# Kernel optimization log

Hardware: AMD Instinct MI355X
Metric: run time of the kernel (lower is better)

The kernel has to match this reference:

```python
import jax, jax.numpy as jnp
import numpy as np

BOS = 1
NUM_LAYERS = 2
HID = 1024
VOCAB = 32000
SEQ = 64


def setup_inputs() -> dict:
    key = jax.random.key(0)
    ks = jax.random.split(key, 16)
    s = 0.02  # weight scale
    return {
        "src": jax.random.randint(ks[0], (SEQ,), 0, VOCAB),
        "tgt": jax.random.randint(ks[1], (SEQ,), 0, VOCAB),
        "emb_enc": jax.random.normal(ks[2], (VOCAB, HID), jnp.float32) * s,
        "enc_Wih": jax.random.normal(ks[3], (NUM_LAYERS, 4 * HID, HID), jnp.float32) * s,
        "enc_Whh": jax.random.normal(ks[4], (NUM_LAYERS, 4 * HID, HID), jnp.float32) * s,
        "enc_bih": jax.random.normal(ks[5], (NUM_LAYERS, 4 * HID), jnp.float32) * s,
        "enc_bhh": jax.random.normal(ks[6], (NUM_LAYERS, 4 * HID), jnp.float32) * s,
        "emb_dec": jax.random.normal(ks[7], (VOCAB, HID), jnp.float32) * s,
        "dec_Wih": jax.random.normal(ks[8], (NUM_LAYERS, 4 * HID, HID), jnp.float32) * s,
        "dec_Whh": jax.random.normal(ks[9], (NUM_LAYERS, 4 * HID, HID), jnp.float32) * s,
        "dec_bih": jax.random.normal(ks[10], (NUM_LAYERS, 4 * HID), jnp.float32) * s,
        "dec_bhh": jax.random.normal(ks[11], (NUM_LAYERS, 4 * HID), jnp.float32) * s,
        "out_W": jax.random.normal(ks[12], (VOCAB, HID), jnp.float32) * s,
        "out_b": jax.random.normal(ks[13], (VOCAB,), jnp.float32) * s,
    }


def _lstm_stack_step(Wih, Whh, bih, bhh, x, h, c):
    # x: [H]; h, c: [L, H]. PyTorch gate order: i, f, g, o.
    new_h, new_c = [], []
    inp = x
    for l in range(Wih.shape[0]):
        g = Wih[l] @ inp + bih[l] + Whh[l] @ h[l] + bhh[l]  # [4H]
        gi, gf, gg, go = jnp.split(g, 4)
        i = jax.nn.sigmoid(gi)
        f = jax.nn.sigmoid(gf)
        cand = jnp.tanh(gg)
        o = jax.nn.sigmoid(go)
        c_l = f * c[l] + i * cand
        h_l = o * jnp.tanh(c_l)
        new_h.append(h_l)
        new_c.append(c_l)
        inp = h_l
    return jnp.stack(new_h), jnp.stack(new_c)


def reference(src, tgt, emb_enc, enc_Wih, enc_Whh, enc_bih, enc_bhh,
              emb_dec, dec_Wih, dec_Whh, dec_bih, dec_bhh, out_W, out_b):
    h0 = jnp.zeros((NUM_LAYERS, HID), jnp.float32)
    c0 = jnp.zeros((NUM_LAYERS, HID), jnp.float32)

    # ---- encoder: seq-major, batch=1 ----
    def enc_step(carry, tok):
        h, c = carry
        x = emb_enc[tok]
        h, c = _lstm_stack_step(enc_Wih, enc_Whh, enc_bih, enc_bhh, x, h, c)
        return (h, c), h[-1]

    (h, c), encoder_outputs = jax.lax.scan(enc_step, (h0, c0), src)

    def dec_step(carry, _):
        h, c, tok = carry
        x = emb_dec[tok]
        h, c = _lstm_stack_step(dec_Wih, dec_Whh, dec_bih, dec_bhh, x, h, c)
        logp = jax.nn.log_softmax(out_W @ h[-1] + out_b)  # [V]
        nxt = jnp.argmax(logp)
        return (h, c, nxt), logp

    tgt_len = tgt.shape[0]
    (_, _, _), dec_logps = jax.lax.scan(
        dec_step, (h, c, jnp.asarray(BOS, src.dtype)), None, length=tgt_len)
    return dec_logps  # [T, V]
```

## Files before the change

### kernel.cpp

```cpp
#include <hip/hip_runtime.h>
#include <math.h>

#define HID    1024
#define G4     4096
#define VOC    32000
#define SEQL   64
#define BOSTOK 1
#define NBLK   256
#define NTHR   1024
#define NWAVES (NTHR / 64)
#define TOTW   (NBLK * NWAVES)

struct P {
  const int*   src;
  const float* embE; const float* eWih; const float* eWhh; const float* ebih; const float* ebhh;
  const float* embD; const float* dWih; const float* dWhh; const float* dbih; const float* dbhh;
  const float* oW;   const float* ob;
  float* out;
  float* ws;
};

__device__ __forceinline__ float gld(const float* p) {
  return __hip_atomic_load((float*)p, __ATOMIC_RELAXED, __HIP_MEMORY_SCOPE_AGENT);
}
__device__ __forceinline__ void gst(float* p, float v) {
  __hip_atomic_store(p, v, __ATOMIC_RELAXED, __HIP_MEMORY_SCOPE_AGENT);
}
__device__ __forceinline__ int gldi(const int* p) {
  return __hip_atomic_load((int*)p, __ATOMIC_RELAXED, __HIP_MEMORY_SCOPE_AGENT);
}
__device__ __forceinline__ void gsti(int* p, int v) {
  __hip_atomic_store(p, v, __ATOMIC_RELAXED, __HIP_MEMORY_SCOPE_AGENT);
}

__device__ __forceinline__ void gridbar(unsigned* cnt, unsigned* gen) {
  __syncthreads();
  if (threadIdx.x == 0) {
    __builtin_amdgcn_s_waitcnt(0);
    unsigned g = __hip_atomic_load(gen, __ATOMIC_RELAXED, __HIP_MEMORY_SCOPE_AGENT);
    unsigned a = __hip_atomic_fetch_add(cnt, 1u, __ATOMIC_ACQ_REL, __HIP_MEMORY_SCOPE_AGENT);
    if (a == NBLK - 1) {
      __hip_atomic_store(cnt, 0u, __ATOMIC_RELAXED, __HIP_MEMORY_SCOPE_AGENT);
      __hip_atomic_fetch_add(gen, 1u, __ATOMIC_RELEASE, __HIP_MEMORY_SCOPE_AGENT);
    } else {
      while (__hip_atomic_load(gen, __ATOMIC_RELAXED, __HIP_MEMORY_SCOPE_AGENT) == g)
        __builtin_amdgcn_s_sleep(8);
      (void)__hip_atomic_load(gen, __ATOMIC_ACQUIRE, __HIP_MEMORY_SCOPE_AGENT);
    }
  }
  __syncthreads();
}

__device__ __forceinline__ float wsum(float v) {
#pragma unroll
  for (int o = 32; o > 0; o >>= 1) v += __shfl_xor(v, o, 64);
  return v;
}

__device__ __forceinline__ float dotg(const float* __restrict__ w, const float* v, int lane) {
  const float4* w4 = (const float4*)w;
  const float4* v4 = (const float4*)v;
  float acc = 0.f;
#pragma unroll
  for (int j = 0; j < 4; ++j) {
    float4 a = w4[lane + 64 * j];
    float4 b = v4[lane + 64 * j];
    acc += a.x * b.x + a.y * b.y + a.z * b.z + a.w * b.w;
  }
  return acc;
}

__device__ __forceinline__ void derive(const float* __restrict__ pa, const float* __restrict__ cin,
                                       float* __restrict__ cout, float* __restrict__ hout, int tid) {
  float gi = gld(pa + tid), gf = gld(pa + HID + tid);
  float gg = gld(pa + 2 * HID + tid), go = gld(pa + 3 * HID + tid);
  float c  = cin ? gld(cin + tid) : 0.f;
  float si = 1.f / (1.f + expf(-gi));
  float sf = 1.f / (1.f + expf(-gf));
  float so = 1.f / (1.f + expf(-go));
  float cn = sf * c + si * tanhf(gg);
  hout[tid] = so * tanhf(cn);
  if (cout) gst(cout + tid, cn);
}

__global__ void init_bar(unsigned* bar) { bar[0] = 0; bar[1] = 0; }

__global__ void __launch_bounds__(NTHR) rnn_all(P p) {
  const int  tid  = threadIdx.x;
  const int  lane = tid & 63;
  const int  wv   = tid >> 6;
  const int  gw   = blockIdx.x * NWAVES + wv;
  const bool b0   = (blockIdx.x == 0);

  unsigned* cnt = (unsigned*)p.ws;
  unsigned* gen = cnt + 1;

  __shared__ __align__(16) float sx[HID];
  __shared__ __align__(16) float sh0[HID];
  __shared__ __align__(16) float sh1[HID];
  __shared__ float rv[NWAVES];
  __shared__ int   ri[NWAVES];
  __shared__ int   stok;

  float* pa0e = p.ws + 64;
  float* pa1e = pa0e + 4 * G4;
  float* pa0d = pa1e + 4 * G4;
  float* pa1d = pa0d + 4 * G4;
  float* c0e  = pa1d + 4 * G4;
  float* c1e  = c0e + 4 * HID;
  float* c0d  = c1e + 4 * HID;
  float* c1d  = c0d + 4 * HID;
  float* B0   = c1d + 4 * HID;
  float* B1   = B0 + G4;
  float* pmv  = B1 + G4;
  int*   pmi  = (int*)(pmv + NBLK);
  float* lsep = (float*)(pmi + NBLK);

  const float* eW0i = p.eWih;  const float* eW1i = p.eWih + (size_t)G4 * HID;
  const float* eW0h = p.eWhh;  const float* eW1h = p.eWhh + (size_t)G4 * HID;
  const float* eb0i = p.ebih;  const float* eb1i = p.ebih + G4;
  const float* eb0h = p.ebhh;  const float* eb1h = p.ebhh + G4;
  const float* dW0i = p.dWih;  const float* dW1i = p.dWih + (size_t)G4 * HID;
  const float* dW0h = p.dWhh;  const float* dW1h = p.dWhh + (size_t)G4 * HID;
  const float* db0i = p.dbih;  const float* db1i = p.dbih + G4;
  const float* db0h = p.dbhh;  const float* db1h = p.dbhh + G4;

  for (int k = 0; k <= SEQL; ++k) {
    if (k < SEQL) {
      int tok = p.src[k];
      sx[tid] = p.embE[(size_t)tok * HID + tid];
    }
    if (k >= 1) {
      derive(pa0e + ((k - 1) & 3) * G4,
             (k >= 2) ? (c0e + ((k - 1) & 3) * HID) : nullptr,
             b0 ? (c0e + (k & 3) * HID) : nullptr, sh0, tid);
    } else sh0[tid] = 0.f;
    if (k >= 2) {
      derive(pa1e + ((k - 2) & 3) * G4,
             (k >= 3) ? (c1e + ((k - 2) & 3) * HID) : nullptr,
             b0 ? (c1e + ((k - 1) & 3) * HID) : nullptr, sh1, tid);
    } else sh1[tid] = 0.f;
    __syncthreads();

    for (int it = gw; it < 2 * G4; it += TOTW) {
      if (it < G4) {
        if (k < SEQL) {
          int r = it;
          float a = dotg(eW0i + (size_t)r * HID, sx, lane) +
                    dotg(eW0h + (size_t)r * HID, sh0, lane);
          float v = wsum(a) + eb0i[r] + eb0h[r];
          if (lane == 0) gst(pa0e + (k & 3) * G4 + r, v);
        }
      } else if (k >= 1) {
        int r = it - G4;
        float a = dotg(eW1i + (size_t)r * HID, sh0, lane) +
                  dotg(eW1h + (size_t)r * HID, sh1, lane);
        float v = wsum(a) + eb1i[r] + eb1h[r];
        if (lane == 0) gst(pa1e + ((k - 1) & 3) * G4 + r, v);
      }
    }
    gridbar(cnt, gen);
  }

  {
    derive(pa0e + (63 & 3) * G4, c0e + (63 & 3) * HID, b0 ? (c0d + 0) : nullptr, sh0, tid);
    derive(pa1e + (63 & 3) * G4, c1e + (63 & 3) * HID, b0 ? (c1d + 0) : nullptr, sh1, tid);
    __syncthreads();
    for (int it = gw; it < 2 * G4; it += TOTW) {
      if (it < G4) {
        int r = it;
        float v = wsum(dotg(dW0h + (size_t)r * HID, sh0, lane)) + db0i[r] + db0h[r];
        if (lane == 0) gst(B0 + r, v);
      } else {
        int r = it - G4;
        float v = wsum(dotg(dW1h + (size_t)r * HID, sh1, lane)) + db1i[r] + db1h[r];
        if (lane == 0) gst(B1 + r, v);
      }
    }
    gridbar(cnt, gen);
  }

  for (int t = 0; t < SEQL; ++t) {
    if (t == 0) {
      if (tid == 0) stok = BOSTOK;
    } else if (wv == 0) {
      float bv = -1e30f; int bi = 0;
#pragma unroll
      for (int j = 0; j < NBLK / 64; ++j) {
        int   idx = lane + 64 * j;
        float v   = gld(pmv + idx);
        int   i2  = gldi(pmi + idx);
        if (v > bv || (v == bv && i2 < bi)) { bv = v; bi = i2; }
      }
#pragma unroll
      for (int o = 32; o > 0; o >>= 1) {
        float v  = __shfl_xor(bv, o, 64);
        int   i2 = __shfl_xor(bi, o, 64);
        if (v > bv || (v == bv && i2 < bi)) { bv = v; bi = i2; }
      }
      if (lane == 0) stok = bi;
    }
    __syncthreads();
    sx[tid] = p.embD[(size_t)stok * HID + tid];
    __syncthreads();
    for (int it = gw; it < G4; it += TOTW) {
      float v = wsum(dotg(dW0i + (size_t)it * HID, sx, lane)) + gld(B0 + it);
      if (lane == 0) gst(pa0d + (t & 3) * G4 + it, v);
    }
    gridbar(cnt, gen);

    derive(pa0d + (t & 3) * G4, c0d + (t & 3) * HID,
           b0 ? (c0d + ((t + 1) & 3) * HID) : nullptr, sh0, tid);
    __syncthreads();
    for (int it = gw; it < G4; it += TOTW) {
      float v = wsum(dotg(dW1i + (size_t)it * HID, sh0, lane)) + gld(B1 + it);
      if (lane == 0) gst(pa1d + (t & 3) * G4 + it, v);
    }
    gridbar(cnt, gen);

    derive(pa1d + (t & 3) * G4, c1d + (t & 3) * HID,
           b0 ? (c1d + ((t + 1) & 3) * HID) : nullptr, sh1, tid);
    __syncthreads();
    float bv = -1e30f; int bi = 0;
    for (int it = gw; it < VOC + 2 * G4; it += TOTW) {
      if (it < VOC) {
        float v = wsum(dotg(p.oW + (size_t)it * HID, sh1, lane)) + p.ob[it];
        if (lane == 0) gst(p.out + (size_t)t * VOC + it, v);
        if (v > bv) { bv = v; bi = it; }
      } else if (it < VOC + G4) {
        int r = it - VOC;
        float v = wsum(dotg(dW0h + (size_t)r * HID, sh0, lane)) + db0i[r] + db0h[r];
        if (lane == 0) gst(B0 + r, v);
      } else {
        int r = it - VOC - G4;
        float v = wsum(dotg(dW1h + (size_t)r * HID, sh1, lane)) + db1i[r] + db1h[r];
        if (lane == 0) gst(B1 + r, v);
      }
    }
    if (lane == 0) { rv[wv] = bv; ri[wv] = bi; }
    __syncthreads();
    if (tid == 0) {
      float v = rv[0]; int i2 = ri[0];
      for (int j = 1; j < NWAVES; ++j)
        if (rv[j] > v || (rv[j] == v && ri[j] < i2)) { v = rv[j]; i2 = ri[j]; }
      gst(pmv + blockIdx.x, v); gsti(pmi + blockIdx.x, i2);
    }
    gridbar(cnt, gen);
  }

  {
    const int row = blockIdx.x >> 2;
    const int seg = blockIdx.x & 3;
    float* base = p.out + (size_t)row * VOC + (size_t)seg * 8000;

    float lm = -1e30f;
    for (int i = tid; i < 8000; i += NTHR) lm = fmaxf(lm, gld(base + i));
#pragma unroll
    for (int o = 32; o > 0; o >>= 1) lm = fmaxf(lm, __shfl_xor(lm, o, 64));
    if (lane == 0) rv[wv] = lm;
    __syncthreads();
    float bm = rv[0];
#pragma unroll
    for (int j = 1; j < NWAVES; ++j) bm = fmaxf(bm, rv[j]);
    float ls = 0.f;
    for (int i = tid; i < 8000; i += NTHR) ls += expf(gld(base + i) - bm);
    ls = wsum(ls);
    __syncthreads();
    if (lane == 0) rv[wv] = ls;
    __syncthreads();
    if (tid == 0) {
      float ss = 0.f;
      for (int j = 0; j < NWAVES; ++j) ss += rv[j];
      gst(lsep + blockIdx.x * 2,     bm);
      gst(lsep + blockIdx.x * 2 + 1, ss);
    }
    gridbar(cnt, gen);

    const float* lp = lsep + (size_t)row * 8;
    float l0 = gld(lp), l2 = gld(lp + 2), l4 = gld(lp + 4), l6 = gld(lp + 6);
    float s1 = gld(lp + 1), s3 = gld(lp + 3), s5 = gld(lp + 5), s7 = gld(lp + 7);
    float M = fmaxf(fmaxf(l0, l2), fmaxf(l4, l6));
    float S = s1 * expf(l0 - M) + s3 * expf(l2 - M) +
              s5 * expf(l4 - M) + s7 * expf(l6 - M);
    float L = M + logf(S);
    for (int i = tid; i < 8000; i += NTHR) base[i] = gld(base + i) - L;
  }
}

extern "C" void kernel_launch(void* const* d_in, const int* in_sizes, int n_in,
                              void* d_out, int out_size, void* d_ws, size_t ws_size,
                              hipStream_t stream) {
  P p;
  p.src  = (const int*)d_in[0];
  p.embE = (const float*)d_in[2];
  p.eWih = (const float*)d_in[3];
  p.eWhh = (const float*)d_in[4];
  p.ebih = (const float*)d_in[5];
  p.ebhh = (const float*)d_in[6];
  p.embD = (const float*)d_in[7];
  p.dWih = (const float*)d_in[8];
  p.dWhh = (const float*)d_in[9];
  p.dbih = (const float*)d_in[10];
  p.dbhh = (const float*)d_in[11];
  p.oW   = (const float*)d_in[12];
  p.ob   = (const float*)d_in[13];
  p.out  = (float*)d_out;
  p.ws   = (float*)d_ws;

  hipLaunchKernelGGL(init_bar, dim3(1), dim3(1), 0, stream, (unsigned*)d_ws);
  void* args[] = { &p };
  hipLaunchCooperativeKernel((const void*)rnn_all, dim3(NBLK), dim3(NTHR), args, 0, stream);
}
```

Before: 8.213 ms.

## Use hierarchical grid barrier and occupancy-sized grid of smaller blocks

Replaces the single-counter grid barrier with a two-level barrier: blocks first arrive at per-group counters, then the last arrival of each group bumps a top-level counter, and release flags are padded across cache lines. Block size drops to 512 threads and the grid is sized from the occupancy query, up to 1024 blocks, so more waves share the weight GEMVs across CUs. The goal is less atomic contention at the roughly 200 grid barriers and higher memory-level parallelism. The cost is more blocks taking part in every barrier, a host-side occupancy query whose result is cached, and generalized softmax segmenting.

```diff
diff --git a/kernel.cpp b/kernel.cpp
--- a/kernel.cpp
+++ b/kernel.cpp
@@ -6,10 +6,10 @@
 #define VOC    32000
 #define SEQL   64
 #define BOSTOK 1
-#define NBLK   256
-#define NTHR   1024
+#define NTHR   512
 #define NWAVES (NTHR / 64)
-#define TOTW   (NBLK * NWAVES)
+#define NGRP   32
+#define BARW   4096
 
 struct P {
   const int*   src;
@@ -33,19 +33,29 @@
   __hip_atomic_store(p, v, __ATOMIC_RELAXED, __HIP_MEMORY_SCOPE_AGENT);
 }
 
-__device__ __forceinline__ void gridbar(unsigned* cnt, unsigned* gen) {
+__device__ __forceinline__ void gridbar(unsigned* bar, unsigned phase, int g, unsigned grpsz) {
   __syncthreads();
   if (threadIdx.x == 0) {
     __builtin_amdgcn_s_waitcnt(0);
-    unsigned g = __hip_atomic_load(gen, __ATOMIC_RELAXED, __HIP_MEMORY_SCOPE_AGENT);
-    unsigned a = __hip_atomic_fetch_add(cnt, 1u, __ATOMIC_ACQ_REL, __HIP_MEMORY_SCOPE_AGENT);
-    if (a == NBLK - 1) {
-      __hip_atomic_store(cnt, 0u, __ATOMIC_RELAXED, __HIP_MEMORY_SCOPE_AGENT);
-      __hip_atomic_fetch_add(gen, 1u, __ATOMIC_RELEASE, __HIP_MEMORY_SCOPE_AGENT);
-    } else {
-      while (__hip_atomic_load(gen, __ATOMIC_RELAXED, __HIP_MEMORY_SCOPE_AGENT) == g)
-        __builtin_amdgcn_s_sleep(8);
-      (void)__hip_atomic_load(gen, __ATOMIC_ACQUIRE, __HIP_MEMORY_SCOPE_AGENT);
+    unsigned* grpc = bar + 64 + 32 * g;
+    unsigned* topc = bar + 32;
+    bool released = false;
+    unsigned a = __hip_atomic_fetch_add(grpc, 1u, __ATOMIC_ACQ_REL, __HIP_MEMORY_SCOPE_AGENT);
+    if (a == phase * grpsz - 1u) {
+      unsigned b = __hip_atomic_fetch_add(topc, 1u, __ATOMIC_ACQ_REL, __HIP_MEMORY_SCOPE_AGENT);
+      if (b == phase * NGRP - 1u) {
+#pragma unroll
+        for (int g2 = 0; g2 < NGRP; ++g2)
+          __hip_atomic_store(bar + 2048 + 32 * g2, phase,
+                             __ATOMIC_RELEASE, __HIP_MEMORY_SCOPE_AGENT);
+        released = true;
+      }
+    }
+    if (!released) {
+      unsigned* gg = bar + 2048 + 32 * g;
+      while (__hip_atomic_load(gg, __ATOMIC_RELAXED, __HIP_MEMORY_SCOPE_AGENT) < phase)
+        __builtin_amdgcn_s_sleep(4);
+      (void)__hip_atomic_load(gg, __ATOMIC_ACQUIRE, __HIP_MEMORY_SCOPE_AGENT);
     }
   }
   __syncthreads();
@@ -72,28 +82,39 @@
 
 __device__ __forceinline__ void derive(const float* __restrict__ pa, const float* __restrict__ cin,
                                        float* __restrict__ cout, float* __restrict__ hout, int tid) {
-  float gi = gld(pa + tid), gf = gld(pa + HID + tid);
-  float gg = gld(pa + 2 * HID + tid), go = gld(pa + 3 * HID + tid);
-  float c  = cin ? gld(cin + tid) : 0.f;
-  float si = 1.f / (1.f + expf(-gi));
-  float sf = 1.f / (1.f + expf(-gf));
-  float so = 1.f / (1.f + expf(-go));
-  float cn = sf * c + si * tanhf(gg);
-  hout[tid] = so * tanhf(cn);
-  if (cout) gst(cout + tid, cn);
-}
-
-__global__ void init_bar(unsigned* bar) { bar[0] = 0; bar[1] = 0; }
-
-__global__ void __launch_bounds__(NTHR) rnn_all(P p) {
-  const int  tid  = threadIdx.x;
-  const int  lane = tid & 63;
-  const int  wv   = tid >> 6;
-  const int  gw   = blockIdx.x * NWAVES + wv;
-  const bool b0   = (blockIdx.x == 0);
-
-  unsigned* cnt = (unsigned*)p.ws;
-  unsigned* gen = cnt + 1;
+  for (int i = tid; i < HID; i += NTHR) {
+    float gi = gld(pa + i), gf = gld(pa + HID + i);
+    float gg = gld(pa + 2 * HID + i), go = gld(pa + 3 * HID + i);
+    float c  = cin ? gld(cin + i) : 0.f;
+    float si = 1.f / (1.f + expf(-gi));
+    float sf = 1.f / (1.f + expf(-gf));
+    float so = 1.f / (1.f + expf(-go));
+    float cn = sf * c + si * tanhf(gg);
+    hout[i] = so * tanhf(cn);
+    if (cout) gst(cout + i, cn);
+  }
+}
+
+__device__ __forceinline__ void zerov(float* h, int tid) {
+  for (int i = tid; i < HID; i += NTHR) h[i] = 0.f;
+}
+
+__global__ void init_bar(unsigned* bar) {
+  for (int i = threadIdx.x; i < BARW; i += 256) bar[i] = 0;
+}
+
+__global__ void __launch_bounds__(NTHR, 8) rnn_all(P p) {
+  const int  tid   = threadIdx.x;
+  const int  lane  = tid & 63;
+  const int  wv    = tid >> 6;
+  const int  nblk  = gridDim.x;
+  const int  totw  = nblk * NWAVES;
+  const int  gw    = blockIdx.x * NWAVES + wv;
+  const int  grp   = blockIdx.x & (NGRP - 1);
+  const unsigned grpsz = (unsigned)(nblk / NGRP);
+  const bool b0    = (blockIdx.x == 0);
+  unsigned   ph    = 0;
+  unsigned*  bar   = (unsigned*)p.ws;
 
   __shared__ __align__(16) float sx[HID];
   __shared__ __align__(16) float sh0[HID];
@@ -102,7 +123,7 @@
   __shared__ int   ri[NWAVES];
   __shared__ int   stok;
 
-  float* pa0e = p.ws + 64;
+  float* pa0e = p.ws + BARW;
   float* pa1e = pa0e + 4 * G4;
   float* pa0d = pa1e + 4 * G4;
   float* pa1d = pa0d + 4 * G4;
@@ -113,8 +134,8 @@
   float* B0   = c1d + 4 * HID;
   float* B1   = B0 + G4;
   float* pmv  = B1 + G4;
-  int*   pmi  = (int*)(pmv + NBLK);
-  float* lsep = (float*)(pmi + NBLK);
+  int*   pmi  = (int*)(pmv + 1024);
+  float* lsep = (float*)(pmi + 1024);
 
   const float* eW0i = p.eWih;  const float* eW1i = p.eWih + (size_t)G4 * HID;
   const float* eW0h = p.eWhh;  const float* eW1h = p.eWhh + (size_t)G4 * HID;
@@ -128,21 +149,21 @@
   for (int k = 0; k <= SEQL; ++k) {
     if (k < SEQL) {
       int tok = p.src[k];
-      sx[tid] = p.embE[(size_t)tok * HID + tid];
+      for (int i = tid; i < HID; i += NTHR) sx[i] = p.embE[(size_t)tok * HID + i];
     }
     if (k >= 1) {
       derive(pa0e + ((k - 1) & 3) * G4,
              (k >= 2) ? (c0e + ((k - 1) & 3) * HID) : nullptr,
              b0 ? (c0e + (k & 3) * HID) : nullptr, sh0, tid);
-    } else sh0[tid] = 0.f;
+    } else zerov(sh0, tid);
     if (k >= 2) {
       derive(pa1e + ((k - 2) & 3) * G4,
              (k >= 3) ? (c1e + ((k - 2) & 3) * HID) : nullptr,
              b0 ? (c1e + ((k - 1) & 3) * HID) : nullptr, sh1, tid);
-    } else sh1[tid] = 0.f;
-    __syncthreads();
-
-    for (int it = gw; it < 2 * G4; it += TOTW) {
+    } else zerov(sh1, tid);
+    __syncthreads();
+
+    for (int it = gw; it < 2 * G4; it += totw) {
       if (it < G4) {
         if (k < SEQL) {
           int r = it;
@@ -159,14 +180,14 @@
         if (lane == 0) gst(pa1e + ((k - 1) & 3) * G4 + r, v);
       }
     }
-    gridbar(cnt, gen);
+    gridbar(bar, ++ph, grp, grpsz);
   }
 
   {
     derive(pa0e + (63 & 3) * G4, c0e + (63 & 3) * HID, b0 ? (c0d + 0) : nullptr, sh0, tid);
     derive(pa1e + (63 & 3) * G4, c1e + (63 & 3) * HID, b0 ? (c1d + 0) : nullptr, sh1, tid);
     __syncthreads();
-    for (int it = gw; it < 2 * G4; it += TOTW) {
+    for (int it = gw; it < 2 * G4; it += totw) {
       if (it < G4) {
         int r = it;
         float v = wsum(dotg(dW0h + (size_t)r * HID, sh0, lane)) + db0i[r] + db0h[r];
@@ -177,7 +198,7 @@
         if (lane == 0) gst(B1 + r, v);
       }
     }
-    gridbar(cnt, gen);
+    gridbar(bar, ++ph, grp, grpsz);
   }
 
   for (int t = 0; t < SEQL; ++t) {
@@ -185,11 +206,9 @@
       if (tid == 0) stok = BOSTOK;
     } else if (wv == 0) {
       float bv = -1e30f; int bi = 0;
-#pragma unroll
-      for (int j = 0; j < NBLK / 64; ++j) {
-        int   idx = lane + 64 * j;
-        float v   = gld(pmv + idx);
-        int   i2  = gldi(pmi + idx);
+      for (int idx = lane; idx < nblk; idx += 64) {
+        float v  = gld(pmv + idx);
+        int   i2 = gldi(pmi + idx);
         if (v > bv || (v == bv && i2 < bi)) { bv = v; bi = i2; }
       }
 #pragma unroll
@@ -201,28 +220,31 @@
       if (lane == 0) stok = bi;
     }
     __syncthreads();
-    sx[tid] = p.embD[(size_t)stok * HID + tid];
-    __syncthreads();
-    for (int it = gw; it < G4; it += TOTW) {
+    {
+      int tok = stok;
+      for (int i = tid; i < HID; i += NTHR) sx[i] = p.embD[(size_t)tok * HID + i];
+    }
+    __syncthreads();
+    for (int it = gw; it < G4; it += totw) {
       float v = wsum(dotg(dW0i + (size_t)it * HID, sx, lane)) + gld(B0 + it);
       if (lane == 0) gst(pa0d + (t & 3) * G4 + it, v);
     }
-    gridbar(cnt, gen);
+    gridbar(bar, ++ph, grp, grpsz);
 
     derive(pa0d + (t & 3) * G4, c0d + (t & 3) * HID,
            b0 ? (c0d + ((t + 1) & 3) * HID) : nullptr, sh0, tid);
     __syncthreads();
-    for (int it = gw; it < G4; it += TOTW) {
+    for (int it = gw; it < G4; it += totw) {
       float v = wsum(dotg(dW1i + (size_t)it * HID, sh0, lane)) + gld(B1 + it);
       if (lane == 0) gst(pa1d + (t & 3) * G4 + it, v);
     }
-    gridbar(cnt, gen);
+    gridbar(bar, ++ph, grp, grpsz);
 
     derive(pa1d + (t & 3) * G4, c1d + (t & 3) * HID,
            b0 ? (c1d + ((t + 1) & 3) * HID) : nullptr, sh1, tid);
     __syncthreads();
     float bv = -1e30f; int bi = 0;
-    for (int it = gw; it < VOC + 2 * G4; it += TOTW) {
+    for (int it = gw; it < VOC + 2 * G4; it += totw) {
       if (it < VOC) {
         float v = wsum(dotg(p.oW + (size_t)it * HID, sh1, lane)) + p.ob[it];
         if (lane == 0) gst(p.out + (size_t)t * VOC + it, v);
@@ -245,16 +267,19 @@
         if (rv[j] > v || (rv[j] == v && ri[j] < i2)) { v = rv[j]; i2 = ri[j]; }
       gst(pmv + blockIdx.x, v); gsti(pmi + blockIdx.x, i2);
     }
-    gridbar(cnt, gen);
+    gridbar(bar, ++ph, grp, grpsz);
   }
 
   {
-    const int row = blockIdx.x >> 2;
-    const int seg = blockIdx.x & 3;
-    float* base = p.out + (size_t)row * VOC + (size_t)seg * 8000;
+    const int spr  = nblk >> 6;
+    const int lg   = (spr == 4) ? 2 : (spr == 8) ? 3 : 4;
+    const int row  = blockIdx.x >> lg;
+    const int seg  = blockIdx.x & (spr - 1);
+    const int slen = VOC >> lg;
+    float* base = p.out + (size_t)row * VOC + (size_t)seg * slen;
 
     float lm = -1e30f;
-    for (int i = tid; i < 8000; i += NTHR) lm = fmaxf(lm, gld(base + i));
+    for (int i = tid; i < slen; i += NTHR) lm = fmaxf(lm, gld(base + i));
 #pragma unroll
     for (int o = 32; o > 0; o >>= 1) lm = fmaxf(lm, __shfl_xor(lm, o, 64));
     if (lane == 0) rv[wv] = lm;
@@ -263,7 +288,7 @@
 #pragma unroll
     for (int j = 1; j < NWAVES; ++j) bm = fmaxf(bm, rv[j]);
     float ls = 0.f;
-    for (int i = tid; i < 8000; i += NTHR) ls += expf(gld(base + i) - bm);
+    for (int i = tid; i < slen; i += NTHR) ls += expf(gld(base + i) - bm);
     ls = wsum(ls);
     __syncthreads();
     if (lane == 0) rv[wv] = ls;
@@ -274,16 +299,15 @@
       gst(lsep + blockIdx.x * 2,     bm);
       gst(lsep + blockIdx.x * 2 + 1, ss);
     }
-    gridbar(cnt, gen);
-
-    const float* lp = lsep + (size_t)row * 8;
-    float l0 = gld(lp), l2 = gld(lp + 2), l4 = gld(lp + 4), l6 = gld(lp + 6);
-    float s1 = gld(lp + 1), s3 = gld(lp + 3), s5 = gld(lp + 5), s7 = gld(lp + 7);
-    float M = fmaxf(fmaxf(l0, l2), fmaxf(l4, l6));
-    float S = s1 * expf(l0 - M) + s3 * expf(l2 - M) +
-              s5 * expf(l4 - M) + s7 * expf(l6 - M);
+    gridbar(bar, ++ph, grp, grpsz);
+
+    const float* lp = lsep + (size_t)row * 2 * spr;
+    float M = -1e30f;
+    for (int j = 0; j < spr; ++j) M = fmaxf(M, gld(lp + 2 * j));
+    float S = 0.f;
+    for (int j = 0; j < spr; ++j) S += gld(lp + 2 * j + 1) * expf(gld(lp + 2 * j) - M);
     float L = M + logf(S);
-    for (int i = tid; i < 8000; i += NTHR) base[i] = gld(base + i) - L;
+    for (int i = tid; i < slen; i += NTHR) base[i] = gld(base + i) - L;
   }
 }
 
@@ -307,7 +331,21 @@
   p.out  = (float*)d_out;
   p.ws   = (float*)d_ws;
 
-  hipLaunchKernelGGL(init_bar, dim3(1), dim3(1), 0, stream, (unsigned*)d_ws);
+  static int g_nblk = 0;
+  if (g_nblk == 0) {
+    int dev = 0;
+    (void)hipGetDevice(&dev);
+    int ncu = 256;
+    (void)hipDeviceGetAttribute(&ncu, hipDeviceAttributeMultiprocessorCount, dev);
+    int maxb = 0;
+    if (hipOccupancyMaxActiveBlocksPerMultiprocessor(&maxb, rnn_all, NTHR, 0) != hipSuccess
+        || maxb < 1)
+      maxb = 1;
+    long cap = (long)maxb * (long)ncu;
+    g_nblk = (cap >= 1024) ? 1024 : (cap >= 512) ? 512 : 256;
+  }
+
+  hipLaunchKernelGGL(init_bar, dim3(1), dim3(256), 0, stream, (unsigned*)d_ws);
   void* args[] = { &p };
-  hipLaunchCooperativeKernel((const void*)rnn_all, dim3(NBLK), dim3(NTHR), args, 0, stream);
-}
+  hipLaunchCooperativeKernel((const void*)rnn_all, dim3(g_nblk), dim3(NTHR), args, 0, stream);
+}
```

Measured after the change: 9.814 ms. 1.19x slower.

## Use fp16 copy of output projection and hierarchical grid barrier

Applied to the files above, without the earlier changes.

Converts the 32000x1024 output weight matrix to fp16 in workspace at kernel start, then computes vocab logits from the half-precision copy with four rows per wave, halving per-step weight bandwidth for the largest matmul. It also replaces the single-counter grid barrier with a two-level grouped barrier and per-group release flags to reduce atomic contention, and sets launch bounds. The fp16 weights introduce rounding that could change argmax tokens and logits, and the conversion costs one full pass over the weights per call.

```diff
diff --git a/kernel.cpp b/kernel.cpp
--- a/kernel.cpp
+++ b/kernel.cpp
@@ -1,4 +1,5 @@
 #include <hip/hip_runtime.h>
+#include <hip/hip_fp16.h>
 #include <math.h>
 
 #define HID    1024
@@ -10,6 +11,11 @@
 #define NTHR   1024
 #define NWAVES (NTHR / 64)
 #define TOTW   (NBLK * NWAVES)
+#define NGRP   32
+#define GRPSZ  (NBLK / NGRP)
+#define BARW   4096
+#define WSBASE 95232
+#define NEEDH  (WSBASE * 4 + (size_t)VOC * HID * 2)
 
 struct P {
   const int*   src;
@@ -18,6 +24,7 @@
   const float* oW;   const float* ob;
   float* out;
   float* ws;
+  int useH;
 };
 
 __device__ __forceinline__ float gld(const float* p) {
@@ -33,19 +40,29 @@
   __hip_atomic_store(p, v, __ATOMIC_RELAXED, __HIP_MEMORY_SCOPE_AGENT);
 }
 
-__device__ __forceinline__ void gridbar(unsigned* cnt, unsigned* gen) {
+__device__ __forceinline__ void gridbar(unsigned* bar, unsigned phase, int g) {
   __syncthreads();
   if (threadIdx.x == 0) {
     __builtin_amdgcn_s_waitcnt(0);
-    unsigned g = __hip_atomic_load(gen, __ATOMIC_RELAXED, __HIP_MEMORY_SCOPE_AGENT);
-    unsigned a = __hip_atomic_fetch_add(cnt, 1u, __ATOMIC_ACQ_REL, __HIP_MEMORY_SCOPE_AGENT);
-    if (a == NBLK - 1) {
-      __hip_atomic_store(cnt, 0u, __ATOMIC_RELAXED, __HIP_MEMORY_SCOPE_AGENT);
-      __hip_atomic_fetch_add(gen, 1u, __ATOMIC_RELEASE, __HIP_MEMORY_SCOPE_AGENT);
-    } else {
-      while (__hip_atomic_load(gen, __ATOMIC_RELAXED, __HIP_MEMORY_SCOPE_AGENT) == g)
-        __builtin_amdgcn_s_sleep(8);
-      (void)__hip_atomic_load(gen, __ATOMIC_ACQUIRE, __HIP_MEMORY_SCOPE_AGENT);
+    unsigned* grpc = bar + 64 + 32 * g;
+    unsigned* topc = bar + 32;
+    bool released = false;
+    unsigned a = __hip_atomic_fetch_add(grpc, 1u, __ATOMIC_ACQ_REL, __HIP_MEMORY_SCOPE_AGENT);
+    if (a == phase * GRPSZ - 1u) {
+      unsigned b = __hip_atomic_fetch_add(topc, 1u, __ATOMIC_ACQ_REL, __HIP_MEMORY_SCOPE_AGENT);
+      if (b == phase * NGRP - 1u) {
+#pragma unroll
+        for (int g2 = 0; g2 < NGRP; ++g2)
+          __hip_atomic_store(bar + 2048 + 32 * g2, phase,
+                             __ATOMIC_RELEASE, __HIP_MEMORY_SCOPE_AGENT);
+        released = true;
+      }
+    }
+    if (!released) {
+      unsigned* gg = bar + 2048 + 32 * g;
+      while (__hip_atomic_load(gg, __ATOMIC_RELAXED, __HIP_MEMORY_SCOPE_AGENT) < phase)
+        __builtin_amdgcn_s_sleep(4);
+      (void)__hip_atomic_load(gg, __ATOMIC_ACQUIRE, __HIP_MEMORY_SCOPE_AGENT);
     }
   }
   __syncthreads();
@@ -67,6 +84,19 @@
     float4 b = v4[lane + 64 * j];
     acc += a.x * b.x + a.y * b.y + a.z * b.z + a.w * b.w;
   }
+  return acc;
+}
+
+__device__ __forceinline__ float dot8(uint4 u, float4 b0, float4 b1) {
+  float2 f; float acc;
+  f = __half22float2(*reinterpret_cast<const __half2*>(&u.x));
+  acc  = f.x * b0.x + f.y * b0.y;
+  f = __half22float2(*reinterpret_cast<const __half2*>(&u.y));
+  acc += f.x * b0.z + f.y * b0.w;
+  f = __half22float2(*reinterpret_cast<const __half2*>(&u.z));
+  acc += f.x * b1.x + f.y * b1.y;
+  f = __half22float2(*reinterpret_cast<const __half2*>(&u.w));
+  acc += f.x * b1.z + f.y * b1.w;
   return acc;
 }
 
@@ -83,17 +113,19 @@
   if (cout) gst(cout + tid, cn);
 }
 
-__global__ void init_bar(unsigned* bar) { bar[0] = 0; bar[1] = 0; }
-
-__global__ void __launch_bounds__(NTHR) rnn_all(P p) {
+__global__ void init_bar(unsigned* bar) {
+  for (int i = threadIdx.x; i < BARW; i += 256) bar[i] = 0;
+}
+
+__global__ void __launch_bounds__(NTHR, 4) rnn_all(P p) {
   const int  tid  = threadIdx.x;
   const int  lane = tid & 63;
   const int  wv   = tid >> 6;
   const int  gw   = blockIdx.x * NWAVES + wv;
+  const int  grp  = blockIdx.x & (NGRP - 1);
   const bool b0   = (blockIdx.x == 0);
-
-  unsigned* cnt = (unsigned*)p.ws;
-  unsigned* gen = cnt + 1;
+  unsigned   ph   = 0;
+  unsigned*  bar  = (unsigned*)p.ws;
 
   __shared__ __align__(16) float sx[HID];
   __shared__ __align__(16) float sh0[HID];
@@ -102,7 +134,7 @@
   __shared__ int   ri[NWAVES];
   __shared__ int   stok;
 
-  float* pa0e = p.ws + 64;
+  float* pa0e = p.ws + BARW;
   float* pa1e = pa0e + 4 * G4;
   float* pa0d = pa1e + 4 * G4;
   float* pa1d = pa0d + 4 * G4;
@@ -115,6 +147,7 @@
   float* pmv  = B1 + G4;
   int*   pmi  = (int*)(pmv + NBLK);
   float* lsep = (float*)(pmi + NBLK);
+  __half* oWh = (__half*)(p.ws + WSBASE);
 
   const float* eW0i = p.eWih;  const float* eW1i = p.eWih + (size_t)G4 * HID;
   const float* eW0h = p.eWhh;  const float* eW1h = p.eWhh + (size_t)G4 * HID;
@@ -124,6 +157,22 @@
   const float* dW0h = p.dWhh;  const float* dW1h = p.dWhh + (size_t)G4 * HID;
   const float* db0i = p.dbih;  const float* db1i = p.dbih + G4;
   const float* db0h = p.dbhh;  const float* db1h = p.dbhh + G4;
+
+  if (p.useH) {
+    const float4* s4 = (const float4*)p.oW;
+    unsigned long long* d8 = (unsigned long long*)oWh;
+    const size_t n4 = (size_t)VOC * HID / 4;
+    for (size_t i = (size_t)blockIdx.x * NTHR + tid; i < n4; i += (size_t)NBLK * NTHR) {
+      float4 f = s4[i];
+      __half2 lo = __float22half2_rn(make_float2(f.x, f.y));
+      __half2 hi = __float22half2_rn(make_float2(f.z, f.w));
+      unsigned long long u =
+          ((unsigned long long)(*reinterpret_cast<unsigned*>(&hi)) << 32) |
+          (unsigned long long)(*reinterpret_cast<unsigned*>(&lo));
+      __hip_atomic_store(d8 + i, u, __ATOMIC_RELAXED, __HIP_MEMORY_SCOPE_AGENT);
+    }
+    gridbar(bar, ++ph, grp);
+  }
 
   for (int k = 0; k <= SEQL; ++k) {
     if (k < SEQL) {
@@ -159,7 +208,7 @@
         if (lane == 0) gst(pa1e + ((k - 1) & 3) * G4 + r, v);
       }
     }
-    gridbar(cnt, gen);
+    gridbar(bar, ++ph, grp);
   }
 
   {
@@ -177,7 +226,7 @@
         if (lane == 0) gst(B1 + r, v);
       }
     }
-    gridbar(cnt, gen);
+    gridbar(bar, ++ph, grp);
   }
 
   for (int t = 0; t < SEQL; ++t) {
@@ -207,7 +256,7 @@
       float v = wsum(dotg(dW0i + (size_t)it * HID, sx, lane)) + gld(B0 + it);
       if (lane == 0) gst(pa0d + (t & 3) * G4 + it, v);
     }
-    gridbar(cnt, gen);
+    gridbar(bar, ++ph, grp);
 
     derive(pa0d + (t & 3) * G4, c0d + (t & 3) * HID,
            b0 ? (c0d + ((t + 1) & 3) * HID) : nullptr, sh0, tid);
@@ -216,25 +265,74 @@
       float v = wsum(dotg(dW1i + (size_t)it * HID, sh0, lane)) + gld(B1 + it);
       if (lane == 0) gst(pa1d + (t & 3) * G4 + it, v);
     }
-    gridbar(cnt, gen);
+    gridbar(bar, ++ph, grp);
 
     derive(pa1d + (t & 3) * G4, c1d + (t & 3) * HID,
            b0 ? (c1d + ((t + 1) & 3) * HID) : nullptr, sh1, tid);
     __syncthreads();
     float bv = -1e30f; int bi = 0;
-    for (int it = gw; it < VOC + 2 * G4; it += TOTW) {
-      if (it < VOC) {
-        float v = wsum(dotg(p.oW + (size_t)it * HID, sh1, lane)) + p.ob[it];
-        if (lane == 0) gst(p.out + (size_t)t * VOC + it, v);
-        if (v > bv) { bv = v; bi = it; }
-      } else if (it < VOC + G4) {
-        int r = it - VOC;
-        float v = wsum(dotg(dW0h + (size_t)r * HID, sh0, lane)) + db0i[r] + db0h[r];
-        if (lane == 0) gst(B0 + r, v);
-      } else {
-        int r = it - VOC - G4;
-        float v = wsum(dotg(dW1h + (size_t)r * HID, sh1, lane)) + db1i[r] + db1h[r];
-        if (lane == 0) gst(B1 + r, v);
+    if (p.useH) {
+      const float4* v4 = (const float4*)sh1;
+      for (int base = 0; base < VOC; base += 4 * TOTW) {
+        int r0 = base + gw;
+        int r1 = r0 + TOTW, r2 = r1 + TOTW, r3 = r2 + TOTW;
+        bool k3 = (r3 < VOC);
+        const uint4* w0 = (const uint4*)(oWh + (size_t)r0 * HID);
+        const uint4* w1 = (const uint4*)(oWh + (size_t)r1 * HID);
+        const uint4* w2 = (const uint4*)(oWh + (size_t)r2 * HID);
+        const uint4* w3 = (const uint4*)(oWh + (size_t)(k3 ? r3 : r0) * HID);
+        float a0 = 0.f, a1 = 0.f, a2 = 0.f, a3 = 0.f;
+#pragma unroll
+        for (int j = 0; j < 2; ++j) {
+          int wi = lane + 64 * j;
+          uint4 u0 = w0[wi], u1 = w1[wi], u2 = w2[wi], u3 = w3[wi];
+          float4 bA = v4[2 * wi], bB = v4[2 * wi + 1];
+          a0 += dot8(u0, bA, bB);
+          a1 += dot8(u1, bA, bB);
+          a2 += dot8(u2, bA, bB);
+          a3 += dot8(u3, bA, bB);
+        }
+        a0 = wsum(a0); a1 = wsum(a1); a2 = wsum(a2); a3 = wsum(a3);
+        float l0 = a0 + p.ob[r0], l1 = a1 + p.ob[r1], l2 = a2 + p.ob[r2];
+        if (lane == 0) {
+          gst(p.out + (size_t)t * VOC + r0, l0);
+          gst(p.out + (size_t)t * VOC + r1, l1);
+          gst(p.out + (size_t)t * VOC + r2, l2);
+        }
+        if (l0 > bv) { bv = l0; bi = r0; }
+        if (l1 > bv) { bv = l1; bi = r1; }
+        if (l2 > bv) { bv = l2; bi = r2; }
+        if (k3) {
+          float l3 = a3 + p.ob[r3];
+          if (lane == 0) gst(p.out + (size_t)t * VOC + r3, l3);
+          if (l3 > bv) { bv = l3; bi = r3; }
+        }
+      }
+      for (int it = gw; it < 2 * G4; it += TOTW) {
+        if (it < G4) {
+          float v = wsum(dotg(dW0h + (size_t)it * HID, sh0, lane)) + db0i[it] + db0h[it];
+          if (lane == 0) gst(B0 + it, v);
+        } else {
+          int r = it - G4;
+          float v = wsum(dotg(dW1h + (size_t)r * HID, sh1, lane)) + db1i[r] + db1h[r];
+          if (lane == 0) gst(B1 + r, v);
+        }
+      }
+    } else {
+      for (int it = gw; it < VOC + 2 * G4; it += TOTW) {
+        if (it < VOC) {
+          float v = wsum(dotg(p.oW + (size_t)it * HID, sh1, lane)) + p.ob[it];
+          if (lane == 0) gst(p.out + (size_t)t * VOC + it, v);
+          if (v > bv) { bv = v; bi = it; }
+        } else if (it < VOC + G4) {
+          int r = it - VOC;
+          float v = wsum(dotg(dW0h + (size_t)r * HID, sh0, lane)) + db0i[r] + db0h[r];
+          if (lane == 0) gst(B0 + r, v);
+        } else {
+          int r = it - VOC - G4;
+          float v = wsum(dotg(dW1h + (size_t)r * HID, sh1, lane)) + db1i[r] + db1h[r];
+          if (lane == 0) gst(B1 + r, v);
+        }
       }
     }
     if (lane == 0) { rv[wv] = bv; ri[wv] = bi; }
@@ -245,7 +343,7 @@
         if (rv[j] > v || (rv[j] == v && ri[j] < i2)) { v = rv[j]; i2 = ri[j]; }
       gst(pmv + blockIdx.x, v); gsti(pmi + blockIdx.x, i2);
     }
-    gridbar(cnt, gen);
+    gridbar(bar, ++ph, grp);
   }
 
   {
@@ -274,7 +372,7 @@
       gst(lsep + blockIdx.x * 2,     bm);
       gst(lsep + blockIdx.x * 2 + 1, ss);
     }
-    gridbar(cnt, gen);
+    gridbar(bar, ++ph, grp);
 
     const float* lp = lsep + (size_t)row * 8;
     float l0 = gld(lp), l2 = gld(lp + 2), l4 = gld(lp + 4), l6 = gld(lp + 6);
@@ -306,8 +404,9 @@
   p.ob   = (const float*)d_in[13];
   p.out  = (float*)d_out;
   p.ws   = (float*)d_ws;
-
-  hipLaunchKernelGGL(init_bar, dim3(1), dim3(1), 0, stream, (unsigned*)d_ws);
+  p.useH = (ws_size >= NEEDH) ? 1 : 0;
+
+  hipLaunchKernelGGL(init_bar, dim3(1), dim3(256), 0, stream, (unsigned*)d_ws);
   void* args[] = { &p };
   hipLaunchCooperativeKernel((const void*)rnn_all, dim3(NBLK), dim3(NTHR), args, 0, stream);
 }
```

New measurement: 7.249 ms. 11.7% less time.
